# Performance work log

Hardware: AMD Instinct MI355X
Metric: run time of the kernel (lower is better)

The kernel has to match this reference:

```python
import jax, jax.numpy as jnp
import numpy as np

MC = 64  # mc_samples; fill=1.0 -> k == k_ball so neighbor ordering is irrelevant


def swish(x):
    return x * jax.nn.sigmoid(x)


def setup_inputs() -> dict:
    key = jax.random.key(0)
    ks = jax.random.split(key, 12)
    bs, n, g_dim = 4, 1024, 6
    c_in = c_out = 256
    H, hid = 8, 16

    def lin(k, i, o):
        return (jax.random.normal(k, (i, o), jnp.float32) / np.sqrt(i).astype(np.float32))

    return {
        "pairwise_g": jax.random.normal(ks[0], (bs, n, n, g_dim), jnp.float32),
        "coset_functions": jax.random.normal(ks[1], (bs, n, c_in), jnp.float32),
        "mask": jax.random.randint(ks[2], (bs, n), 0, 2) > 0,
        # per-head location-kernel MLP (MultiheadWeightNet: g_dim -> hid -> hid -> 1)
        "loc_W1": jax.random.normal(ks[3], (H, g_dim, hid), jnp.float32) / np.sqrt(g_dim).astype(np.float32),
        "loc_b1": jnp.zeros((H, hid), jnp.float32),
        "loc_W2": jax.random.normal(ks[4], (H, hid, hid), jnp.float32) / np.sqrt(hid).astype(np.float32),
        "loc_b2": jnp.zeros((H, hid), jnp.float32),
        "loc_W3": jax.random.normal(ks[5], (H, hid, 1), jnp.float32) / np.sqrt(hid).astype(np.float32),
        "loc_b3": jnp.zeros((H, 1), jnp.float32),
        # DotProductKernel projections
        "Wq": lin(ks[6], c_in, c_in), "bq": jnp.zeros((c_in,), jnp.float32),
        "Wk": lin(ks[7], c_in, c_in), "bk": jnp.zeros((c_in,), jnp.float32),
        # value (input_linear) and output projections
        "W_in": lin(ks[8], c_in, c_out), "b_in": jnp.zeros((c_out,), jnp.float32),
        "W_out": lin(ks[9], c_out, c_out), "b_out": jnp.zeros((c_out,), jnp.float32),
    }


def reference(pairwise_g, coset_functions, mask, loc_W1, loc_b1, loc_W2, loc_b2,
              loc_W3, loc_b3, Wq, bq, Wk, bk, W_in, b_in, W_out, b_out):
    bs, n, _, g_dim = pairwise_g.shape
    c_in = coset_functions.shape[-1]
    H = loc_W1.shape[0]
    dh = c_in // H
    b_idx = jnp.arange(bs)[:, None, None]

    # --- neighbourhood extraction: topk (smallest) group distances, masked keys pushed far away
    dists = jnp.linalg.norm(pairwise_g, axis=-1)                  # (b,n,n)
    dists = jnp.where(mask[:, None, :], dists, jnp.float32(1e8))
    _, nbhd_idx = jax.lax.top_k(-dists, MC)                       # (b,n,m) nearest MC keys
    nbhd_g = jnp.take_along_axis(pairwise_g, nbhd_idx[..., None], axis=2)  # (b,n,m,g)
    nbhd_mask = mask[b_idx, nbhd_idx]                             # (b,n,m)

    # --- location kernel: per-head MLP on gathered pairwise group elements
    h = swish(jnp.einsum('bnmg,hgk->bnmhk', nbhd_g, loc_W1) + loc_b1)
    h = swish(jnp.einsum('bnmhk,hkl->bnmhl', h, loc_W2) + loc_b2)
    loc = swish(jnp.einsum('bnmhk,hko->bnmho', h, loc_W3) + loc_b3)[..., 0]  # (b,n,m,H)

    # --- feature kernel: dot-product scores on gathered keys
    q = (coset_functions @ Wq + bq).reshape(bs, n, H, dh)
    k = (coset_functions @ Wk + bk).reshape(bs, n, H, dh)
    k_nbhd = k[b_idx, nbhd_idx]                                   # (b,n,m,H,dh)
    feat = jnp.einsum('bnhd,bnmhd->bnmh', q, k_nbhd) / np.sqrt(dh).astype(np.float32)

    # --- masked softmax over the neighbourhood dim (dim 2)
    scores = jnp.where(nbhd_mask[..., None], loc + feat, jnp.float32(-1e38))
    attn = jax.nn.softmax(scores, axis=2)                         # (b,n,m,H)

    # --- value projection + sparse attention (equivalent to the dense scatter+matmul,
    #     since topk neighbour indices are unique per query)
    v = (coset_functions @ W_in + b_in).reshape(bs, n, H, dh)
    v_nbhd = v[b_idx, nbhd_idx]                                   # (b,n,m,H,dh)
    out = jnp.einsum('bnmh,bnmhd->bnhd', attn, v_nbhd).reshape(bs, n, H * dh)
    out = out @ W_out + b_out
    return (pairwise_g, out, mask)
```

## Files before the change

kernel.cpp:

```cpp
#include <hip/hip_runtime.h>
#include <stdint.h>

#define BS 4
#define NN 1024
#define GD 6
#define CIN 256
#define NH 8
#define DH 32
#define HID 16
#define MCS 64

#define PG_ELEMS (BS*NN*NN*GD)
#define OUT_OFF  PG_ELEMS
#define MASK_OFF (PG_ELEMS + BS*NN*CIN)

typedef float vfloat4 __attribute__((ext_vector_type(4)));
typedef float vfloat2 __attribute__((ext_vector_type(2)));
typedef unsigned vuint4 __attribute__((ext_vector_type(4)));

#if __has_builtin(__builtin_amdgcn_rcpf)
__device__ __forceinline__ float fast_rcp(float x) { return __builtin_amdgcn_rcpf(x); }
#else
__device__ __forceinline__ float fast_rcp(float x) { return 1.0f / x; }
#endif
#if __has_builtin(__builtin_amdgcn_exp2f)
__device__ __forceinline__ float fast_exp2(float x) { return __builtin_amdgcn_exp2f(x); }
#else
__device__ __forceinline__ float fast_exp2(float x) { return exp2f(x); }
#endif
#define LOG2E 1.44269504088896340736f

__device__ __forceinline__ float swishf(float x) {
    return x * fast_rcp(1.0f + fast_exp2(x * -LOG2E));
}

template<int RPB>
__global__ __launch_bounds__(256) void gemm3(const float* __restrict__ X,
    const float* __restrict__ W0, const float* __restrict__ B0, float* __restrict__ D0,
    const float* __restrict__ W1, const float* __restrict__ B1, float* __restrict__ D1,
    const float* __restrict__ W2, const float* __restrict__ B2, float* __restrict__ D2)
{
    const float* W; const float* Bv; float* D;
    if (blockIdx.y == 0)      { W = W0; Bv = B0; D = D0; }
    else if (blockIdx.y == 1) { W = W1; Bv = B1; D = D1; }
    else                      { W = W2; Bv = B2; D = D2; }
    const int tid = threadIdx.x;
    const int c4  = tid & 63;
    const int rg  = tid >> 6;
    const int r0  = blockIdx.x * RPB;
    constexpr int RG = RPB / 4;

    __shared__ float xsT[CIN][RPB + 4];
    {
        float tmp[RPB];
        #pragma unroll
        for (int r = 0; r < RPB; ++r) tmp[r] = X[(size_t)(r0 + r)*CIN + tid];
        #pragma unroll
        for (int j = 0; j < RPB/4; ++j)
            *(vfloat4*)&xsT[tid][4*j] = (vfloat4){tmp[4*j+0], tmp[4*j+1], tmp[4*j+2], tmp[4*j+3]};
    }
    __syncthreads();

    vfloat4 acc[RG];
    #pragma unroll
    for (int r = 0; r < RG; ++r) acc[r] = (vfloat4){0.f,0.f,0.f,0.f};
    const vfloat4* W4 = (const vfloat4*)W;
    #pragma unroll 4
    for (int k = 0; k < CIN; ++k) {
        vfloat4 w = W4[(size_t)k*64 + c4];
        if constexpr (RG == 4) {
            vfloat4 xr = *(const vfloat4*)&xsT[k][rg*4];
            acc[0] += xr.x * w;
            acc[1] += xr.y * w;
            acc[2] += xr.z * w;
            acc[3] += xr.w * w;
        } else {
            vfloat2 xr = *(const vfloat2*)&xsT[k][rg*2];
            acc[0] += xr.x * w;
            acc[1] += xr.y * w;
        }
    }
    vfloat4 bb = ((const vfloat4*)Bv)[c4];
    vfloat4* D4 = (vfloat4*)D;
    const size_t rbase = (size_t)(r0 + rg*RG);
    #pragma unroll
    for (int r = 0; r < RG; ++r) D4[(rbase + r)*64 + c4] = acc[r] + bb;
}

__global__ __launch_bounds__(256, 8) void attn_topk(
    const float* __restrict__ pg, const int* __restrict__ mask,
    const float* __restrict__ lW1g, const float* __restrict__ lb1g,
    const float* __restrict__ lW2g, const float* __restrict__ lb2g,
    const float* __restrict__ lW3g, const float* __restrict__ lb3g,
    const float* __restrict__ Q, const float* __restrict__ Kc, const float* __restrict__ Vc,
    float* __restrict__ O, float* __restrict__ pg_out, float* __restrict__ mask_out)
{
    const int i = blockIdx.x, b = blockIdx.y, tid = threadIdx.x;
    const int lane = tid & 63;

    __shared__ __align__(16) unsigned selbuf[512];
    __shared__ float sg[MCS*7];
    __shared__ int nj[MCS];
    __shared__ __align__(16) unsigned joff[MCS];
    __shared__ vfloat4 obuf[4][64];
    __shared__ unsigned wsum[4];
    __shared__ unsigned sel_bin, sel_need, s_cnt, s_eqcnt;

    float (*sc)[NH]   = (float (*)[NH])selbuf;
    unsigned* eqlist  = selbuf + 256;

    const int* mrow = mask + b*NN;
    if (tid == 0) { mask_out[b*NN + i] = mrow[i] ? 1.0f : 0.0f; s_cnt = 0; s_eqcnt = 0; }

    const size_t rowoff = (size_t)(b*NN + i) * (NN*GD);
    const vfloat4* src4 = (const vfloat4*)(pg + rowoff);
    vfloat4* dst4 = (vfloat4*)(pg_out + rowoff);

    vfloat4 q4 = ((const vfloat4*)Q)[(size_t)(b*NN + i)*64 + (tid & 63)];
    const int4 mv = ((const int4*)mrow)[tid];

    const vfloat4* gg = src4 + tid*6;
    vfloat4 g0 = gg[0], g1 = gg[1], g2 = gg[2], g3 = gg[3], g4 = gg[4], g5 = gg[5];
    float rv[4][6];
    rv[0][0]=g0.x; rv[0][1]=g0.y; rv[0][2]=g0.z; rv[0][3]=g0.w; rv[0][4]=g1.x; rv[0][5]=g1.y;
    rv[1][0]=g1.z; rv[1][1]=g1.w; rv[1][2]=g2.x; rv[1][3]=g2.y; rv[1][4]=g2.z; rv[1][5]=g2.w;
    rv[2][0]=g3.x; rv[2][1]=g3.y; rv[2][2]=g3.z; rv[2][3]=g3.w; rv[2][4]=g4.x; rv[2][5]=g4.y;
    rv[3][0]=g4.z; rv[3][1]=g4.w; rv[3][2]=g5.x; rv[3][3]=g5.y; rv[3][4]=g5.z; rv[3][5]=g5.w;
    const int vb[4] = { mv.x, mv.y, mv.z, mv.w };
    unsigned key[4];
    #pragma unroll
    for (int r = 0; r < 4; ++r) {
        float d2 = rv[r][0]*rv[r][0] + rv[r][1]*rv[r][1] + rv[r][2]*rv[r][2]
                 + rv[r][3]*rv[r][3] + rv[r][4]*rv[r][4] + rv[r][5]*rv[r][5];
        key[r] = __float_as_uint(vb[r] ? d2 : 1e30f);
    }

    selbuf[tid] = 0;
    selbuf[tid + 256] = 0;
    __syncthreads();

    unsigned prefix = 0;
    int need = MCS;
    for (int level = 0; level < 4; ++level) {
        const int shift = 24 - 8*level;
        unsigned* hist = selbuf + ((level & 1) << 8);
        if (level == 0) {
            #pragma unroll
            for (int r = 0; r < 4; ++r) {
                unsigned d = key[r] >> 24;
                unsigned long long todo = __ballot(true);
                while (todo) {
                    int leader = (int)(__ffsll((unsigned long long)todo) - 1);
                    unsigned dl = __shfl(d, leader);
                    unsigned long long match = __ballot(d == dl);
                    if (lane == leader) atomicAdd(&hist[dl], (unsigned)__popcll(match));
                    todo &= ~match;
                }
            }
        } else {
            const unsigned pmask = 0xFFFFFFFFu << (shift + 8);
            #pragma unroll
            for (int r = 0; r < 4; ++r)
                if ((key[r] & pmask) == prefix)
                    atomicAdd(&hist[(key[r] >> shift) & 0xFFu], 1u);
        }
        __syncthreads();
        unsigned own = hist[tid];
        hist[tid] = 0;
        unsigned v = own;
        #pragma unroll
        for (int off = 1; off < 64; off <<= 1) {
            unsigned nv = __shfl_up(v, off);
            if (lane >= off) v += nv;
        }
        if (lane == 63) wsum[tid >> 6] = v;
        __syncthreads();
        unsigned basec = 0;
        for (int w = 0; w < (tid >> 6); ++w) basec += wsum[w];
        unsigned incl = v + basec;
        unsigned excl = incl - own;
        if (excl < (unsigned)need && (unsigned)need <= incl) {
            sel_bin = (unsigned)tid;
            sel_need = (unsigned)need - excl;
        }
        __syncthreads();
        prefix |= (sel_bin << shift);
        need = (int)sel_need;
    }
    const unsigned T = prefix;
    const int needT = need;

    #pragma unroll
    for (int r = 0; r < 4; ++r) {
        unsigned kk = key[r];
        int j = tid*4 + r;
        if (kk < T) {
            unsigned p = atomicAdd(&s_cnt, 1u);
            nj[p] = j | (vb[r] ? 0 : (int)0x80000000);
            #pragma unroll
            for (int g = 0; g < GD; ++g) sg[p*7 + g] = rv[r][g];
        } else if (kk == T) {
            unsigned e = atomicAdd(&s_eqcnt, 1u);
            if (e < 64) eqlist[e] = (unsigned)j;
        }
    }
    __syncthreads();
    const int cbase = (int)s_cnt;
    if (tid == 0) {
        int ec = (int)s_eqcnt; if (ec > 64) ec = 64;
        for (int s2 = 0; s2 < needT; ++s2) {
            int bi = -1, bj = 0x7FFFFFFF;
            for (int e = 0; e < ec; ++e) {
                int jj = (int)eqlist[e];
                if (jj < bj) { bj = jj; bi = e; }
            }
            if (bi >= 0) {
                eqlist[bi] = 0x7FFFFFFFu;
                nj[cbase + s2] = bj | (mrow[bj] ? 0 : (int)0x80000000);
            }
        }
    }
    __syncthreads();
    #pragma unroll
    for (int r = 0; r < 4; ++r) {
        if (key[r] == T) {
            int j = tid*4 + r;
            for (int s2 = 0; s2 < needT; ++s2)
                if ((nj[cbase + s2] & 0x7FFFFFFF) == j) {
                    #pragma unroll
                    for (int g = 0; g < GD; ++g) sg[(cbase + s2)*7 + g] = rv[r][g];
                }
        }
    }
    if (tid < MCS) joff[tid] = ((unsigned)(b*NN + (nj[tid] & 0x7FFFFFFF))) << 6;
    __syncthreads();

    const int q = tid & 63;
    const int p = tid >> 6;
    const int hh = q >> 3;
    q4 *= 0.17677669529663688f;
    const vfloat4* Kc4 = (const vfloat4*)Kc;
    float pack0 = 0.f, pack1 = 0.f;
    {
        const vuint4* jo4 = (const vuint4*)(joff + (p << 4));
        vuint4 oa = jo4[0], ob = jo4[1], oc = jo4[2], od = jo4[3];
        #define FEAT_ONE(OFF, RR, PACK) do { \
            vfloat4 kv = Kc4[(OFF) + (unsigned)q]; \
            float d = q4.x * kv.x; \
            d = fmaf(q4.y, kv.y, d); \
            d = fmaf(q4.z, kv.z, d); \
            d = fmaf(q4.w, kv.w, d); \
            d += __shfl_xor(d, 1); \
            d += __shfl_xor(d, 2); \
            d += __shfl_xor(d, 4); \
            if ((q & 7) == (RR)) (PACK) = d; \
        } while (0)
        FEAT_ONE(oa.x, 0, pack0); FEAT_ONE(oa.y, 1, pack0);
        FEAT_ONE(oa.z, 2, pack0); FEAT_ONE(oa.w, 3, pack0);
        FEAT_ONE(ob.x, 4, pack0); FEAT_ONE(ob.y, 5, pack0);
        FEAT_ONE(ob.z, 6, pack0); FEAT_ONE(ob.w, 7, pack0);
        FEAT_ONE(oc.x, 0, pack1); FEAT_ONE(oc.y, 1, pack1);
        FEAT_ONE(oc.z, 2, pack1); FEAT_ONE(oc.w, 3, pack1);
        FEAT_ONE(od.x, 4, pack1); FEAT_ONE(od.y, 5, pack1);
        FEAT_ONE(od.z, 6, pack1); FEAT_ONE(od.w, 7, pack1);
        #undef FEAT_ONE
    }

    #pragma unroll
    for (int t = 0; t < 6; ++t) {
        vfloat4 v = src4[tid + 256*t];
        __builtin_nontemporal_store(v, &dst4[tid + 256*t]);
    }

    __builtin_amdgcn_s_setprio(1);
    #pragma unroll
    for (int pass = 0; pass < 2; ++pass) {
        const int h = __builtin_amdgcn_readfirstlane((tid >> 6) + pass*4);
        const int m = lane;
        const float* W1h = lW1g + h*(GD*HID);
        const float* B1h = lb1g + h*HID;
        const float* W2h = lW2g + h*(HID*HID);
        const float* B2h = lb2g + h*HID;
        const float* W3h = lW3g + h*HID;
        float gv[GD];
        #pragma unroll
        for (int g = 0; g < GD; ++g) gv[g] = sg[m*7 + g];
        float h1[HID];
        #pragma unroll
        for (int kk = 0; kk < HID; ++kk) {
            float a = B1h[kk];
            #pragma unroll
            for (int g = 0; g < GD; ++g) a += gv[g] * W1h[g*HID + kk];
            h1[kk] = swishf(a);
        }
        float h2[HID];
        #pragma unroll
        for (int l = 0; l < HID; ++l) {
            float a = B2h[l];
            #pragma unroll
            for (int kk = 0; kk < HID; ++kk) a += h1[kk] * W2h[kk*HID + l];
            h2[l] = swishf(a);
        }
        float a3 = lb3g[h];
        #pragma unroll
        for (int kk = 0; kk < HID; ++kk) a3 += h2[kk] * W3h[kk];
        sc[m][h] = (nj[m] < 0) ? -1e38f : swishf(a3);
    }
    __syncthreads();

    {
        float* scf = (float*)selbuf;
        const int a0 = p*128 + ((q & 7) << 3) + (q >> 3);
        scf[a0]      += pack0;
        scf[a0 + 64] += pack1;
    }
    __syncthreads();

    #pragma unroll
    for (int pass = 0; pass < 2; ++pass) {
        int h = (tid >> 6) + pass*4;
        float s = sc[lane][h];
        float mx = s;
        #pragma unroll
        for (int off = 32; off; off >>= 1) mx = fmaxf(mx, __shfl_xor(mx, off));
        float e = fast_exp2((s - mx) * LOG2E);
        float sum = e;
        #pragma unroll
        for (int off = 32; off; off >>= 1) sum += __shfl_xor(sum, off);
        sc[lane][h] = e * fast_rcp(sum);
    }
    __syncthreads();

    {
        const vfloat4* Vc4 = (const vfloat4*)Vc;
        const vuint4* jo4 = (const vuint4*)(joff + (p << 4));
        vuint4 oa = jo4[0], ob = jo4[1], oc = jo4[2], od = jo4[3];
        vfloat4 acc = (vfloat4){0.f,0.f,0.f,0.f};
        #define OUT_ONE(OFF, MM) do { \
            float a = sc[MM][hh]; \
            vfloat4 v4 = Vc4[(OFF) + (unsigned)q]; \
            acc += a * v4; \
        } while (0)
        const int mb = p << 4;
        OUT_ONE(oa.x, mb+0);  OUT_ONE(oa.y, mb+1);  OUT_ONE(oa.z, mb+2);  OUT_ONE(oa.w, mb+3);
        OUT_ONE(ob.x, mb+4);  OUT_ONE(ob.y, mb+5);  OUT_ONE(ob.z, mb+6);  OUT_ONE(ob.w, mb+7);
        OUT_ONE(oc.x, mb+8);  OUT_ONE(oc.y, mb+9);  OUT_ONE(oc.z, mb+10); OUT_ONE(oc.w, mb+11);
        OUT_ONE(od.x, mb+12); OUT_ONE(od.y, mb+13); OUT_ONE(od.z, mb+14); OUT_ONE(od.w, mb+15);
        #undef OUT_ONE
        __builtin_amdgcn_s_setprio(0);
        obuf[p][q] = acc;
    }
    __syncthreads();
    {
        const float* ob = (const float*)obuf;
        float s = ob[tid] + ob[256 + tid] + ob[512 + tid] + ob[768 + tid];
        O[(size_t)(b*NN + i)*CIN + tid] = s;
    }
}

extern "C" void kernel_launch(void* const* d_in, const int* in_sizes, int n_in,
                              void* d_out, int out_size, void* d_ws, size_t ws_size,
                              hipStream_t stream) {
    const float* pg   = (const float*)d_in[0];
    const float* x    = (const float*)d_in[1];
    const int*   mask = (const int*)d_in[2];
    const float* lW1  = (const float*)d_in[3];
    const float* lb1  = (const float*)d_in[4];
    const float* lW2  = (const float*)d_in[5];
    const float* lb2  = (const float*)d_in[6];
    const float* lW3  = (const float*)d_in[7];
    const float* lb3  = (const float*)d_in[8];
    const float* Wq   = (const float*)d_in[9];
    const float* bq   = (const float*)d_in[10];
    const float* Wk   = (const float*)d_in[11];
    const float* bk   = (const float*)d_in[12];
    const float* Wv   = (const float*)d_in[13];
    const float* bv   = (const float*)d_in[14];
    const float* Wo   = (const float*)d_in[15];
    const float* bo   = (const float*)d_in[16];

    float* out = (float*)d_out;
    float* Q  = (float*)d_ws;
    float* Kc = Q  + (size_t)BS*NN*CIN;
    float* Vc = Kc + (size_t)BS*NN*CIN;
    float* O  = Vc + (size_t)BS*NN*CIN;

    gemm3<16><<<dim3(BS*NN/16, 3), 256, 0, stream>>>(x, Wq, bq, Q, Wk, bk, Kc, Wv, bv, Vc);
    attn_topk<<<dim3(NN, BS), 256, 0, stream>>>(pg, mask, lW1, lb1, lW2, lb2, lW3, lb3,
                                                Q, Kc, Vc, O, out, out + MASK_OFF);
    gemm3<8><<<dim3(BS*NN/8, 1), 256, 0, stream>>>(O, Wo, bo, out + OUT_OFF,
                                                   Wo, bo, out + OUT_OFF,
                                                   Wo, bo, out + OUT_OFF);
}
```

Before: 359.5 us.

## Early-exit radix select with wave rank pass; move pg copy and feature dot after MLP

The radix top-k selection now stops as soon as the selected bin holds at most 64 candidates. Those candidates are gathered into shared memory and a single wave ranks them directly, which skips the remaining histogram levels and their barriers. The pairwise_g passthrough copy is issued at kernel start, and the dot-product feature pass now runs after the location MLP, adding straight into the score array instead of holding packed registers. This shortens the register live range across the MLP at the cost of an extra serial ranking loop and some extra barriers.

```diff
diff --git a/kernel.cpp b/kernel.cpp
--- a/kernel.cpp
+++ b/kernel.cpp
@@ -104,21 +104,26 @@
     __shared__ __align__(16) unsigned joff[MCS];
     __shared__ vfloat4 obuf[4][64];
     __shared__ unsigned wsum[4];
-    __shared__ unsigned sel_bin, sel_need, s_cnt, s_eqcnt;
+    __shared__ unsigned sel_bin, sel_need, sel_cnt2, s_cnt, s_eqcnt, s_cand;
 
     float (*sc)[NH]   = (float (*)[NH])selbuf;
+    unsigned* hist    = selbuf;
     unsigned* eqlist  = selbuf + 256;
 
     const int* mrow = mask + b*NN;
-    if (tid == 0) { mask_out[b*NN + i] = mrow[i] ? 1.0f : 0.0f; s_cnt = 0; s_eqcnt = 0; }
+    if (tid == 0) { mask_out[b*NN + i] = mrow[i] ? 1.0f : 0.0f; s_cand = 0; }
 
     const size_t rowoff = (size_t)(b*NN + i) * (NN*GD);
     const vfloat4* src4 = (const vfloat4*)(pg + rowoff);
     vfloat4* dst4 = (vfloat4*)(pg_out + rowoff);
-
+    #pragma unroll
+    for (int t = 0; t < 6; ++t) {
+        vfloat4 v = src4[tid + 256*t];
+        __builtin_nontemporal_store(v, &dst4[tid + 256*t]);
+    }
     vfloat4 q4 = ((const vfloat4*)Q)[(size_t)(b*NN + i)*64 + (tid & 63)];
+
     const int4 mv = ((const int4*)mrow)[tid];
-
     const vfloat4* gg = src4 + tid*6;
     vfloat4 g0 = gg[0], g1 = gg[1], g2 = gg[2], g3 = gg[3], g4 = gg[4], g5 = gg[5];
     float rv[4][6];
@@ -135,15 +140,14 @@
         key[r] = __float_as_uint(vb[r] ? d2 : 1e30f);
     }
 
-    selbuf[tid] = 0;
-    selbuf[tid + 256] = 0;
-    __syncthreads();
-
     unsigned prefix = 0;
     int need = MCS;
+    unsigned T = 0;
+    int needT = 0;
     for (int level = 0; level < 4; ++level) {
         const int shift = 24 - 8*level;
-        unsigned* hist = selbuf + ((level & 1) << 8);
+        hist[tid] = 0;
+        __syncthreads();
         if (level == 0) {
             #pragma unroll
             for (int r = 0; r < 4; ++r) {
@@ -166,7 +170,6 @@
         }
         __syncthreads();
         unsigned own = hist[tid];
-        hist[tid] = 0;
         unsigned v = own;
         #pragma unroll
         for (int off = 1; off < 64; off <<= 1) {
@@ -180,16 +183,47 @@
         unsigned incl = v + basec;
         unsigned excl = incl - own;
         if (excl < (unsigned)need && (unsigned)need <= incl) {
-            sel_bin = (unsigned)tid;
+            sel_bin  = (unsigned)tid;
             sel_need = (unsigned)need - excl;
+            sel_cnt2 = own;
         }
         __syncthreads();
         prefix |= (sel_bin << shift);
         need = (int)sel_need;
-    }
-    const unsigned T = prefix;
-    const int needT = need;
-
+        if (level == 3) { T = prefix; needT = need; break; }
+        const int bincnt = (int)sel_cnt2;
+        if (bincnt <= 64) {
+            const unsigned pmask = 0xFFFFFFFFu << shift;
+            unsigned* ckey = selbuf + 256;
+            #pragma unroll
+            for (int r = 0; r < 4; ++r) {
+                if ((key[r] & pmask) == prefix) {
+                    unsigned u = atomicAdd(&s_cand, 1u);
+                    ckey[u] = key[r];
+                }
+            }
+            __syncthreads();
+            if (tid < 64) {
+                unsigned myk = (tid < bincnt) ? ckey[tid] : 0xFFFFFFFFu;
+                int rr = 0, ee = 0;
+                for (int t = 0; t < bincnt; ++t) {
+                    unsigned kt = __shfl(myk, t);
+                    rr += (kt <  myk) ? 1 : 0;
+                    ee += (kt == myk) ? 1 : 0;
+                }
+                if (tid < bincnt && rr < need && need <= rr + ee) {
+                    sel_bin  = myk;
+                    sel_need = (unsigned)(need - rr);
+                }
+            }
+            __syncthreads();
+            T = sel_bin; needT = (int)sel_need;
+            break;
+        }
+    }
+
+    if (tid == 0) { s_cnt = 0; s_eqcnt = 0; }
+    __syncthreads();
     #pragma unroll
     for (int r = 0; r < 4; ++r) {
         unsigned kk = key[r];
@@ -235,43 +269,6 @@
     if (tid < MCS) joff[tid] = ((unsigned)(b*NN + (nj[tid] & 0x7FFFFFFF))) << 6;
     __syncthreads();
 
-    const int q = tid & 63;
-    const int p = tid >> 6;
-    const int hh = q >> 3;
-    q4 *= 0.17677669529663688f;
-    const vfloat4* Kc4 = (const vfloat4*)Kc;
-    float pack0 = 0.f, pack1 = 0.f;
-    {
-        const vuint4* jo4 = (const vuint4*)(joff + (p << 4));
-        vuint4 oa = jo4[0], ob = jo4[1], oc = jo4[2], od = jo4[3];
-        #define FEAT_ONE(OFF, RR, PACK) do { \
-            vfloat4 kv = Kc4[(OFF) + (unsigned)q]; \
-            float d = q4.x * kv.x; \
-            d = fmaf(q4.y, kv.y, d); \
-            d = fmaf(q4.z, kv.z, d); \
-            d = fmaf(q4.w, kv.w, d); \
-            d += __shfl_xor(d, 1); \
-            d += __shfl_xor(d, 2); \
-            d += __shfl_xor(d, 4); \
-            if ((q & 7) == (RR)) (PACK) = d; \
-        } while (0)
-        FEAT_ONE(oa.x, 0, pack0); FEAT_ONE(oa.y, 1, pack0);
-        FEAT_ONE(oa.z, 2, pack0); FEAT_ONE(oa.w, 3, pack0);
-        FEAT_ONE(ob.x, 4, pack0); FEAT_ONE(ob.y, 5, pack0);
-        FEAT_ONE(ob.z, 6, pack0); FEAT_ONE(ob.w, 7, pack0);
-        FEAT_ONE(oc.x, 0, pack1); FEAT_ONE(oc.y, 1, pack1);
-        FEAT_ONE(oc.z, 2, pack1); FEAT_ONE(oc.w, 3, pack1);
-        FEAT_ONE(od.x, 4, pack1); FEAT_ONE(od.y, 5, pack1);
-        FEAT_ONE(od.z, 6, pack1); FEAT_ONE(od.w, 7, pack1);
-        #undef FEAT_ONE
-    }
-
-    #pragma unroll
-    for (int t = 0; t < 6; ++t) {
-        vfloat4 v = src4[tid + 256*t];
-        __builtin_nontemporal_store(v, &dst4[tid + 256*t]);
-    }
-
     __builtin_amdgcn_s_setprio(1);
     #pragma unroll
     for (int pass = 0; pass < 2; ++pass) {
@@ -308,11 +305,32 @@
     }
     __syncthreads();
 
-    {
-        float* scf = (float*)selbuf;
-        const int a0 = p*128 + ((q & 7) << 3) + (q >> 3);
-        scf[a0]      += pack0;
-        scf[a0 + 64] += pack1;
+    const int q = tid & 63;
+    const int p = tid >> 6;
+    const int hh = q >> 3;
+    q4 *= 0.17677669529663688f;
+    const vfloat4* Kc4 = (const vfloat4*)Kc;
+    const vuint4* jo4 = (const vuint4*)(joff + (p << 4));
+    #pragma unroll
+    for (int mg = 0; mg < 4; ++mg) {
+        vuint4 o4 = jo4[mg];
+        vfloat4 kv0 = Kc4[o4.x + (unsigned)q];
+        vfloat4 kv1 = Kc4[o4.y + (unsigned)q];
+        vfloat4 kv2 = Kc4[o4.z + (unsigned)q];
+        vfloat4 kv3 = Kc4[o4.w + (unsigned)q];
+        const int mb = (p << 4) + (mg << 2);
+        #define FEAT_RED(KV, RR) do { \
+            float d = q4.x * (KV).x; \
+            d = fmaf(q4.y, (KV).y, d); \
+            d = fmaf(q4.z, (KV).z, d); \
+            d = fmaf(q4.w, (KV).w, d); \
+            d += __shfl_xor(d, 1); \
+            d += __shfl_xor(d, 2); \
+            d += __shfl_xor(d, 4); \
+            if ((q & 7) == 0) sc[mb + (RR)][hh] += d; \
+        } while (0)
+        FEAT_RED(kv0, 0); FEAT_RED(kv1, 1); FEAT_RED(kv2, 2); FEAT_RED(kv3, 3);
+        #undef FEAT_RED
     }
     __syncthreads();
 
@@ -333,20 +351,24 @@
 
     {
         const vfloat4* Vc4 = (const vfloat4*)Vc;
-        const vuint4* jo4 = (const vuint4*)(joff + (p << 4));
-        vuint4 oa = jo4[0], ob = jo4[1], oc = jo4[2], od = jo4[3];
         vfloat4 acc = (vfloat4){0.f,0.f,0.f,0.f};
-        #define OUT_ONE(OFF, MM) do { \
-            float a = sc[MM][hh]; \
-            vfloat4 v4 = Vc4[(OFF) + (unsigned)q]; \
-            acc += a * v4; \
-        } while (0)
-        const int mb = p << 4;
-        OUT_ONE(oa.x, mb+0);  OUT_ONE(oa.y, mb+1);  OUT_ONE(oa.z, mb+2);  OUT_ONE(oa.w, mb+3);
-        OUT_ONE(ob.x, mb+4);  OUT_ONE(ob.y, mb+5);  OUT_ONE(ob.z, mb+6);  OUT_ONE(ob.w, mb+7);
-        OUT_ONE(oc.x, mb+8);  OUT_ONE(oc.y, mb+9);  OUT_ONE(oc.z, mb+10); OUT_ONE(oc.w, mb+11);
-        OUT_ONE(od.x, mb+12); OUT_ONE(od.y, mb+13); OUT_ONE(od.z, mb+14); OUT_ONE(od.w, mb+15);
-        #undef OUT_ONE
+        #pragma unroll
+        for (int mg = 0; mg < 4; ++mg) {
+            vuint4 o4 = jo4[mg];
+            vfloat4 v0 = Vc4[o4.x + (unsigned)q];
+            vfloat4 v1 = Vc4[o4.y + (unsigned)q];
+            vfloat4 v2 = Vc4[o4.z + (unsigned)q];
+            vfloat4 v3 = Vc4[o4.w + (unsigned)q];
+            const int mb = (p << 4) + (mg << 2);
+            float a0 = sc[mb + 0][hh];
+            float a1 = sc[mb + 1][hh];
+            float a2 = sc[mb + 2][hh];
+            float a3 = sc[mb + 3][hh];
+            acc += a0 * v0;
+            acc += a1 * v1;
+            acc += a2 * v2;
+            acc += a3 * v3;
+        }
         __builtin_amdgcn_s_setprio(0);
         obuf[p][q] = acc;
     }
```

New measurement: 329.5 us. 8.4% less time.
